# Kernel optimization log

Hardware: AMD Instinct MI355X
Metric: run time of the kernel (lower is better)

Reference implementation:

```python
import jax, jax.numpy as jnp
import numpy as np
from jax import lax

ITER_TIME = 32
DECAY = 0.9


def setup_inputs() -> dict:
    key = jax.random.key(0)
    k1, k2, k3, k4 = jax.random.split(key, 4)
    B, D_in, N, D_out = 256, 1024, 4096, 256
    s_in = 1.0 / np.sqrt(D_in)
    s_rec = 0.5 / np.sqrt(N)  # keep recurrence stable
    s_out = 1.0 / np.sqrt(N)
    return {
        "x": jax.random.normal(k1, (B, D_in), dtype=jnp.float32),
        "W_i": jax.random.normal(k2, (D_in, N), dtype=jnp.float32) * s_in,
        "b": jnp.zeros((N,), dtype=jnp.float32),
        "W_r": jax.random.normal(k3, (N, N), dtype=jnp.float32) * s_rec,
        "W_f": jax.random.normal(k4, (N, D_out), dtype=jnp.float32) * s_out,
    }


def reference(x, W_i, b, W_r, W_f):
    # prep_input_endure: constant input drive each timestep
    i_ = x @ W_i + b  # [B, N]
    u0 = jnp.zeros_like(i_)
    r0 = jnp.zeros_like(i_)

    def step(carry, _):
        u, r = carry
        u_new = DECAY * u + i_ + r           # leaky integration of drive + recurrent feedback
        a = jax.nn.relu(u_new)               # firing rate / surrogate spike
        r_new = a @ W_r                      # recurrent N->N feedback
        f = a @ W_f                          # readout N->Y
        return (u_new, r_new), (f, u_new)

    (_, _), (fs, us) = lax.scan(step, (u0, r0), None, length=ITER_TIME)
    output = jnp.transpose(fs, (1, 0, 2))  # [B, T, output_num]
    act = jnp.transpose(us, (1, 0, 2))     # [B, T, N_num]
    return output, act
```

## Files before the change

### kernel.cpp

```cpp
#include <hip/hip_runtime.h>
#include <hip/hip_bf16.h>

#define ITER_TIME 32
#define DECAY 0.9f

typedef __attribute__((ext_vector_type(8))) short short8;
typedef __attribute__((ext_vector_type(4))) float f32x4;
typedef __attribute__((ext_vector_type(4))) short short4v;
typedef unsigned short ushort_t;
typedef unsigned int u32;

__device__ __forceinline__ void gload16(const ushort_t* g, ushort_t* l) {
    __builtin_amdgcn_global_load_lds(
        (const __attribute__((address_space(1))) u32*)g,
        (__attribute__((address_space(3))) u32*)l, 16, 0, 0);
}

__global__ void conv_f32_bf16(const float* __restrict__ in,
                              __hip_bfloat16* __restrict__ out, int n) {
    int i = blockIdx.x * 256 + threadIdx.x;
    if (i < n) out[i] = __float2bfloat16(in[i]);
}

__global__ void transpose_f32_bf16(const float* __restrict__ in,
                                   __hip_bfloat16* __restrict__ out, int R,
                                   int C) {
    __shared__ float tile[32][33];
    int tx = threadIdx.x, ty = threadIdx.y;
    size_t x = blockIdx.x * 32 + tx;
    size_t y = blockIdx.y * 32 + ty;
    tile[ty][tx] = in[y * C + x];
    __syncthreads();
    size_t ox = blockIdx.y * 32 + tx;
    size_t oy = blockIdx.x * 32 + ty;
    out[oy * R + ox] = __float2bfloat16(tile[tx][ty]);
}

__global__ __launch_bounds__(256)
void gemm_wi(const ushort_t* __restrict__ A,
             const ushort_t* __restrict__ BT,
             const float* __restrict__ bias, float* __restrict__ i_,
             float* __restrict__ u, __hip_bfloat16* __restrict__ a0,
             float* __restrict__ act, int K) {
    __shared__ __attribute__((aligned(16))) ushort_t As[2][128 * 64];
    __shared__ __attribute__((aligned(16))) ushort_t Bs[2][128 * 64];

    int m0 = blockIdx.x * 128;
    int by = blockIdx.y;
    const ushort_t* Bsrc = BT + (size_t)by * 128 * K;

    int t = threadIdx.x;
    int wave = t >> 6, lane = t & 63;
    int quad = lane >> 4, l16 = lane & 15;
    int wm = (wave >> 1) * 64, wn = (wave & 1) * 64;

    int lr = lane >> 3;
    int lcol = ((lane & 7) ^ lr) << 3;
    const ushort_t* aBase = A + (size_t)(m0 + wave * 32 + lr) * K + lcol;
    const ushort_t* bBase = Bsrc + (size_t)(wave * 32 + lr) * K + lcol;

    f32x4 acc[4][4];
#pragma unroll
    for (int i = 0; i < 4; i++)
#pragma unroll
        for (int j = 0; j < 4; j++) acc[i][j] = (f32x4){0.f, 0.f, 0.f, 0.f};

    int nt = K >> 6;
    int swz = (l16 & 7) << 3;

    auto stage = [&](int buf, int kk) {
#pragma unroll
        for (int i = 0; i < 4; ++i) {
            gload16(aBase + (size_t)(i * 8) * K + kk,
                    &As[buf][(wave * 4 + i) * 512]);
            gload16(bBase + (size_t)(i * 8) * K + kk,
                    &Bs[buf][(wave * 4 + i) * 512]);
        }
    };

    stage(0, 0);
    __syncthreads();
    int cur = 0;
    for (int it = 0; it < nt; ++it) {
        if (it + 1 < nt) stage(cur ^ 1, (it + 1) * 64);
#pragma unroll
        for (int kstep = 0; kstep < 2; ++kstep) {
            int ko = kstep * 32 + quad * 8;
            int pc = ko ^ swz;
            short8 af[4], bfr[4];
#pragma unroll
            for (int i = 0; i < 4; i++)
                af[i] = *(const short8*)&As[cur][(wm + i * 16 + l16) * 64 + pc];
#pragma unroll
            for (int j = 0; j < 4; j++)
                bfr[j] = *(const short8*)&Bs[cur][(wn + j * 16 + l16) * 64 + pc];
#pragma unroll
            for (int i = 0; i < 4; i++)
#pragma unroll
                for (int j = 0; j < 4; j++)
                    acc[i][j] = __builtin_amdgcn_mfma_f32_16x16x32_bf16(
                        af[i], bfr[j], acc[i][j], 0, 0, 0);
        }
        __syncthreads();
        cur ^= 1;
    }

#pragma unroll
    for (int i = 0; i < 4; i++)
#pragma unroll
        for (int j = 0; j < 4; j++) {
            int gcol = by * 128 + wn + j * 16 + l16;
#pragma unroll
            for (int rr = 0; rr < 4; ++rr) {
                int grow = m0 + wm + i * 16 + quad * 4 + rr;
                size_t p = (size_t)grow * 4096 + gcol;
                float iv = acc[i][j][rr] + bias[gcol];
                i_[p] = iv;
                u[p] = iv;
                __builtin_nontemporal_store(
                    iv, &act[(size_t)grow * (ITER_TIME * 4096) + gcol]);
                float ar = iv > 0.f ? iv : 0.f;
                a0[p] = __float2bfloat16(ar);
            }
        }
}

template <int ONLY_F>
__global__ __launch_bounds__(256)
void gemm_step(const ushort_t* __restrict__ A,
               const ushort_t* __restrict__ BT,
               float* __restrict__ rp,
               float* __restrict__ fp) {
    const int K = 4096, klen = 2048;
    __shared__ __attribute__((aligned(16))) ushort_t As[2][128 * 64];
    __shared__ __attribute__((aligned(16))) ushort_t Bs[2][32 * 64];

    int blk = blockIdx.x;
    int by, ks, m;
    if (ONLY_F) {
        by = 128 + (blk >> 2);
        int w = blk & 3;
        m = w & 1;
        ks = w >> 1;
    } else {
        int x = blk & 15, g = blk >> 4;
        int xcd = x & 7;
        m = x >> 3;
        int pair = g * 8 + xcd;
        by = pair % 136;
        ks = pair / 136;
    }
    int m0 = m * 128;
    const ushort_t* Bsrc = BT + (size_t)by * 32 * K;

    int tid = threadIdx.x;
    int wave = tid >> 6, lane = tid & 63;
    int quad = lane >> 4, l16 = lane & 15;

    int lr = lane >> 3;
    int lcol = ((lane & 7) ^ lr) << 3;
    const ushort_t* aBase = A + (size_t)(m0 + wave * 32 + lr) * K + lcol;
    const ushort_t* bBase = Bsrc + (size_t)(wave * 8 + lr) * K + lcol;

    f32x4 acc[2][2];
#pragma unroll
    for (int i = 0; i < 2; i++)
#pragma unroll
        for (int j = 0; j < 2; j++) acc[i][j] = (f32x4){0.f, 0.f, 0.f, 0.f};

    const int k0 = ks * klen;
    const int nt = klen >> 6;
    int swz = (l16 & 7) << 3;

    auto stage = [&](int buf, int kk) {
#pragma unroll
        for (int i = 0; i < 4; ++i)
            gload16(aBase + (size_t)(i * 8) * K + kk,
                    &As[buf][(wave * 4 + i) * 512]);
        gload16(bBase + kk, &Bs[buf][wave * 512]);
    };

    stage(0, k0);
    __syncthreads();
    int cur = 0;
    for (int it = 0; it < nt; ++it) {
        if (it + 1 < nt) stage(cur ^ 1, k0 + (it + 1) * 64);
#pragma unroll
        for (int kstep = 0; kstep < 2; ++kstep) {
            int ko = kstep * 32 + quad * 8;
            int pc = ko ^ swz;
            short8 af[2], bfr[2];
#pragma unroll
            for (int i = 0; i < 2; i++)
                af[i] = *(const short8*)&As[cur][(wave * 32 + i * 16 + l16) * 64 +
                                                 pc];
#pragma unroll
            for (int j = 0; j < 2; j++)
                bfr[j] = *(const short8*)&Bs[cur][(j * 16 + l16) * 64 + pc];
#pragma unroll
            for (int i = 0; i < 2; i++)
#pragma unroll
                for (int j = 0; j < 2; j++)
                    acc[i][j] = __builtin_amdgcn_mfma_f32_16x16x32_bf16(
                        af[i], bfr[j], acc[i][j], 0, 0, 0);
        }
        __syncthreads();
        cur ^= 1;
    }

#pragma unroll
    for (int i = 0; i < 2; i++)
#pragma unroll
        for (int j = 0; j < 2; j++) {
            int cl = j * 16 + l16;
#pragma unroll
            for (int rr = 0; rr < 4; ++rr) {
                int grow = m0 + wave * 32 + i * 16 + quad * 4 + rr;
                float v = acc[i][j][rr];
                if (by < 128) {
                    rp[(size_t)ks * (256 * 4096) + (size_t)grow * 4096 +
                       by * 32 + cl] = v;
                } else {
                    fp[(size_t)ks * (256 * 256) + (size_t)grow * 256 +
                       (by - 128) * 32 + cl] = v;
                }
            }
        }
}

__global__ void elem_step(const float* __restrict__ i_, float* __restrict__ u,
                          __hip_bfloat16* __restrict__ a,
                          const float* __restrict__ rp,
                          const float* __restrict__ fp,
                          float* __restrict__ out, float* __restrict__ act,
                          int t, int fonly) {
    const int NU = 256 * 4096, NU4 = NU / 4;
    const int NF = 256 * 256, NF4 = NF / 4;
    int raw = blockIdx.x * 256 + threadIdx.x;
    int id4 = fonly ? (NU4 + raw) : raw;
    if (id4 >= NU4 + NF4) return;
    if (id4 < NU4) {
        int id = id4 * 4;
        int b = id >> 12, n = id & 4095;
        f32x4 s = *(const f32x4*)&i_[id] + *(const f32x4*)&rp[id] +
                  *(const f32x4*)&rp[NU + id];
        f32x4 un = DECAY * *(const f32x4*)&u[id] + s;
        *(f32x4*)&u[id] = un;
        short4v av;
#pragma unroll
        for (int j = 0; j < 4; ++j) {
            float ar = un[j] > 0.f ? un[j] : 0.f;
            __hip_bfloat16 h = __float2bfloat16(ar);
            av[j] = *(short*)&h;
        }
        *(short4v*)&a[id] = av;
        __builtin_nontemporal_store(
            un, (f32x4*)&act[(size_t)b * (ITER_TIME * 4096) +
                             (size_t)t * 4096 + n]);
    } else {
        int id2 = (id4 - NU4) * 4;
        int b = id2 >> 8, d = id2 & 255;
        f32x4 fv = *(const f32x4*)&fp[id2] + *(const f32x4*)&fp[NF + id2];
        __builtin_nontemporal_store(
            fv, (f32x4*)&out[(size_t)b * (ITER_TIME * 256) +
                             (size_t)(t - 1) * 256 + d]);
    }
}

extern "C" void kernel_launch(void* const* d_in, const int* in_sizes, int n_in,
                              void* d_out, int out_size, void* d_ws,
                              size_t ws_size, hipStream_t stream) {
    const float* x = (const float*)d_in[0];
    const float* Wi = (const float*)d_in[1];
    const float* bb = (const float*)d_in[2];
    const float* Wr = (const float*)d_in[3];
    const float* Wf = (const float*)d_in[4];

    float* out = (float*)d_out;
    float* act = out + (size_t)256 * ITER_TIME * 256;

    char* ws = (char*)d_ws;
    __hip_bfloat16* BT = (__hip_bfloat16*)(ws + 0x0);
    float* i_ = (float*)(ws + 0x2200000);
    float* u = (float*)(ws + 0x2600000);
    __hip_bfloat16* a = (__hip_bfloat16*)(ws + 0x2A00000);
    float* rp = (float*)(ws + 0x2C00000);
    float* fp = (float*)(ws + 0x3400000);
    __hip_bfloat16* xb = (__hip_bfloat16*)(ws + 0x3480000);
    __hip_bfloat16* WiT = (__hip_bfloat16*)(ws + 0x3500000);

    conv_f32_bf16<<<1024, 256, 0, stream>>>(x, xb, 256 * 1024);
    dim3 tb(32, 32);
    transpose_f32_bf16<<<dim3(128, 32), tb, 0, stream>>>(Wi, WiT, 1024, 4096);
    transpose_f32_bf16<<<dim3(128, 128), tb, 0, stream>>>(Wr, BT, 4096, 4096);
    transpose_f32_bf16<<<dim3(8, 128), tb, 0, stream>>>(
        Wf, BT + (size_t)4096 * 4096, 4096, 256);

    gemm_wi<<<dim3(2, 32), 256, 0, stream>>>((const ushort_t*)xb,
                                             (const ushort_t*)WiT, bb, i_, u,
                                             a, act, 1024);

    for (int t = 0; t < ITER_TIME - 1; ++t) {
        gemm_step<0><<<544, 256, 0, stream>>>((const ushort_t*)a,
                                              (const ushort_t*)BT, rp, fp);
        elem_step<<<1088, 256, 0, stream>>>(i_, u, a, rp, fp, out, act, t + 1,
                                            0);
    }
    gemm_step<1><<<32, 256, 0, stream>>>((const ushort_t*)a,
                                         (const ushort_t*)BT, rp, fp);
    elem_step<<<64, 256, 0, stream>>>(i_, u, a, rp, fp, out, act, ITER_TIME,
                                      1);
}
```

Before: 1.218 ms.

## Widen recurrent GEMM tile to 128x64 and use 4-way split-K

The per-step GEMM tile grows from 128x32 to 128x64 with a 2x2 wave arrangement, and split-K goes from 2 to 4 slices. The grid size and block-to-XCD mapping stay the same. Each block now stages less A and B data relative to its output, which cuts global and LDS load traffic per MFMA. In exchange there are four partial-sum buffers instead of two, so the elementwise step reads more data, now through non-temporal loads. Workspace buffers are re-laid out, and the prep buffers WiT and xb are aliased onto the partial-sum regions.

Result: faster. 1.110 ms (-8.9%).

```diff
diff --git a/kernel.cpp b/kernel.cpp
--- a/kernel.cpp
+++ b/kernel.cpp
@@ -131,40 +131,41 @@
                const ushort_t* __restrict__ BT,
                float* __restrict__ rp,
                float* __restrict__ fp) {
-    const int K = 4096, klen = 2048;
+    const int K = 4096, klen = 1024;
     __shared__ __attribute__((aligned(16))) ushort_t As[2][128 * 64];
-    __shared__ __attribute__((aligned(16))) ushort_t Bs[2][32 * 64];
+    __shared__ __attribute__((aligned(16))) ushort_t Bs[2][64 * 64];
 
     int blk = blockIdx.x;
-    int by, ks, m;
+    int by, w;
     if (ONLY_F) {
-        by = 128 + (blk >> 2);
-        int w = blk & 3;
-        m = w & 1;
-        ks = w >> 1;
+        by = 64 + (blk >> 3);
+        w = blk & 7;
+    } else if (blk < 512) {
+        int xcd = blk & 7, bg = (blk >> 3) & 7;
+        w = blk >> 6;
+        by = xcd + 8 * bg;
     } else {
-        int x = blk & 15, g = blk >> 4;
-        int xcd = x & 7;
-        m = x >> 3;
-        int pair = g * 8 + xcd;
-        by = pair % 136;
-        ks = pair / 136;
-    }
+        int idx = blk - 512;
+        by = 64 + (idx >> 3);
+        w = idx & 7;
+    }
+    int m = w & 1, ks = w >> 1;
     int m0 = m * 128;
-    const ushort_t* Bsrc = BT + (size_t)by * 32 * K;
+    const ushort_t* Bsrc = BT + (size_t)by * 64 * K;
 
     int tid = threadIdx.x;
     int wave = tid >> 6, lane = tid & 63;
     int quad = lane >> 4, l16 = lane & 15;
+    int wm = (wave >> 1) * 64, wn = (wave & 1) * 32;
 
     int lr = lane >> 3;
     int lcol = ((lane & 7) ^ lr) << 3;
     const ushort_t* aBase = A + (size_t)(m0 + wave * 32 + lr) * K + lcol;
-    const ushort_t* bBase = Bsrc + (size_t)(wave * 8 + lr) * K + lcol;
-
-    f32x4 acc[2][2];
-#pragma unroll
-    for (int i = 0; i < 2; i++)
+    const ushort_t* bBase = Bsrc + (size_t)(wave * 16 + lr) * K + lcol;
+
+    f32x4 acc[4][2];
+#pragma unroll
+    for (int i = 0; i < 4; i++)
 #pragma unroll
         for (int j = 0; j < 2; j++) acc[i][j] = (f32x4){0.f, 0.f, 0.f, 0.f};
 
@@ -177,7 +178,10 @@
         for (int i = 0; i < 4; ++i)
             gload16(aBase + (size_t)(i * 8) * K + kk,
                     &As[buf][(wave * 4 + i) * 512]);
-        gload16(bBase + kk, &Bs[buf][wave * 512]);
+#pragma unroll
+        for (int i = 0; i < 2; ++i)
+            gload16(bBase + (size_t)(i * 8) * K + kk,
+                    &Bs[buf][(wave * 2 + i) * 512]);
     };
 
     stage(0, k0);
@@ -189,16 +193,15 @@
         for (int kstep = 0; kstep < 2; ++kstep) {
             int ko = kstep * 32 + quad * 8;
             int pc = ko ^ swz;
-            short8 af[2], bfr[2];
-#pragma unroll
-            for (int i = 0; i < 2; i++)
-                af[i] = *(const short8*)&As[cur][(wave * 32 + i * 16 + l16) * 64 +
-                                                 pc];
+            short8 af[4], bfr[2];
+#pragma unroll
+            for (int i = 0; i < 4; i++)
+                af[i] = *(const short8*)&As[cur][(wm + i * 16 + l16) * 64 + pc];
 #pragma unroll
             for (int j = 0; j < 2; j++)
-                bfr[j] = *(const short8*)&Bs[cur][(j * 16 + l16) * 64 + pc];
-#pragma unroll
-            for (int i = 0; i < 2; i++)
+                bfr[j] = *(const short8*)&Bs[cur][(wn + j * 16 + l16) * 64 + pc];
+#pragma unroll
+            for (int i = 0; i < 4; i++)
 #pragma unroll
                 for (int j = 0; j < 2; j++)
                     acc[i][j] = __builtin_amdgcn_mfma_f32_16x16x32_bf16(
@@ -209,20 +212,20 @@
     }
 
 #pragma unroll
-    for (int i = 0; i < 2; i++)
+    for (int i = 0; i < 4; i++)
 #pragma unroll
         for (int j = 0; j < 2; j++) {
-            int cl = j * 16 + l16;
+            int cl = wn + j * 16 + l16;
 #pragma unroll
             for (int rr = 0; rr < 4; ++rr) {
-                int grow = m0 + wave * 32 + i * 16 + quad * 4 + rr;
+                int grow = m0 + wm + i * 16 + quad * 4 + rr;
                 float v = acc[i][j][rr];
-                if (by < 128) {
+                if (by < 64) {
                     rp[(size_t)ks * (256 * 4096) + (size_t)grow * 4096 +
-                       by * 32 + cl] = v;
+                       by * 64 + cl] = v;
                 } else {
                     fp[(size_t)ks * (256 * 256) + (size_t)grow * 256 +
-                       (by - 128) * 32 + cl] = v;
+                       (by - 64) * 64 + cl] = v;
                 }
             }
         }
@@ -242,8 +245,11 @@
     if (id4 < NU4) {
         int id = id4 * 4;
         int b = id >> 12, n = id & 4095;
-        f32x4 s = *(const f32x4*)&i_[id] + *(const f32x4*)&rp[id] +
-                  *(const f32x4*)&rp[NU + id];
+        f32x4 s = *(const f32x4*)&i_[id];
+#pragma unroll
+        for (int k = 0; k < 4; ++k)
+            s += __builtin_nontemporal_load(
+                (const f32x4*)&rp[(size_t)k * NU + id]);
         f32x4 un = DECAY * *(const f32x4*)&u[id] + s;
         *(f32x4*)&u[id] = un;
         short4v av;
@@ -260,7 +266,11 @@
     } else {
         int id2 = (id4 - NU4) * 4;
         int b = id2 >> 8, d = id2 & 255;
-        f32x4 fv = *(const f32x4*)&fp[id2] + *(const f32x4*)&fp[NF + id2];
+        f32x4 fv = {0.f, 0.f, 0.f, 0.f};
+#pragma unroll
+        for (int k = 0; k < 4; ++k)
+            fv += __builtin_nontemporal_load(
+                (const f32x4*)&fp[(size_t)k * NF + id2]);
         __builtin_nontemporal_store(
             fv, (f32x4*)&out[(size_t)b * (ITER_TIME * 256) +
                              (size_t)(t - 1) * 256 + d]);
@@ -285,9 +295,9 @@
     float* u = (float*)(ws + 0x2600000);
     __hip_bfloat16* a = (__hip_bfloat16*)(ws + 0x2A00000);
     float* rp = (float*)(ws + 0x2C00000);
-    float* fp = (float*)(ws + 0x3400000);
-    __hip_bfloat16* xb = (__hip_bfloat16*)(ws + 0x3480000);
-    __hip_bfloat16* WiT = (__hip_bfloat16*)(ws + 0x3500000);
+    float* fp = (float*)(ws + 0x3C00000);
+    __hip_bfloat16* WiT = (__hip_bfloat16*)(ws + 0x2C00000);
+    __hip_bfloat16* xb = (__hip_bfloat16*)(ws + 0x3C00000);
 
     conv_f32_bf16<<<1024, 256, 0, stream>>>(x, xb, 256 * 1024);
     dim3 tb(32, 32);
```
